# Kernel optimization log

Hardware: AMD Instinct MI355X
Metric: run time of the kernel (lower is better)

## Reference

```python
import jax, jax.numpy as jnp
import numpy as np

N_NODES = 100000
N_EDGES = 400000
N_GRAPHS = 1000
DIM = 5
N_OUT = 2
EPS = 1e-5


def _linear_params(key, fan_in, fan_out):
    kw, kb = jax.random.split(key)
    s = 1.0 / np.sqrt(fan_in)
    w = jax.random.uniform(kw, (fan_in, fan_out), minval=-s, maxval=s, dtype=jnp.float32)
    b = jax.random.uniform(kb, (fan_out,), minval=-s, maxval=s, dtype=jnp.float32)
    return w, b


def _gn_params(c):
    # rows: [weight, bias, mean_scale] as in PyG GraphNorm init (1, 0, 1)
    return jnp.stack([jnp.ones((c,)), jnp.zeros((c,)), jnp.ones((c,))], axis=0).astype(jnp.float32)


def setup_inputs() -> dict:
    key = jax.random.key(0)
    ks = jax.random.split(key, 16)
    x = jax.random.normal(ks[0], (N_NODES, DIM), dtype=jnp.float32)
    edge_index = jax.random.randint(ks[1], (2, N_EDGES), 0, N_NODES, dtype=jnp.int64)
    batch = jnp.sort(jax.random.randint(ks[2], (N_NODES,), 0, N_GRAPHS, dtype=jnp.int64))
    c1_w1, c1_b1 = _linear_params(ks[3], 2 * DIM, 128)
    c1_w2, c1_b2 = _linear_params(ks[4], 128, 128)
    c1_w3, c1_b3 = _linear_params(ks[5], 128, 128)
    c2_w1, c2_b1 = _linear_params(ks[6], 2 * 128, 256)
    c2_w2, c2_b2 = _linear_params(ks[7], 256, 256)
    c3_w1, c3_b1 = _linear_params(ks[8], 2 * 256, 256)
    lin_w1, lin_b1 = _linear_params(ks[9], 256, 256)
    lin_w2, lin_b2 = _linear_params(ks[10], 256, N_OUT)
    return {
        "x": x, "edge_index": edge_index, "batch": batch,
        "c1_w1": c1_w1, "c1_b1": c1_b1, "c1_gn1": _gn_params(128),
        "c1_w2": c1_w2, "c1_b2": c1_b2, "c1_gn2": _gn_params(128),
        "c1_w3": c1_w3, "c1_b3": c1_b3, "c1_gn3": _gn_params(128),
        "c2_w1": c2_w1, "c2_b1": c2_b1, "c2_gn1": _gn_params(256),
        "c2_w2": c2_w2, "c2_b2": c2_b2, "c2_gn2": _gn_params(256),
        "c3_w1": c3_w1, "c3_b1": c3_b1, "c3_gn1": _gn_params(256),
        "lin_w1": lin_w1, "lin_b1": lin_b1, "lin_w2": lin_w2, "lin_b2": lin_b2,
    }


def _graph_norm(h, p):
    # PyG GraphNorm with batch=None: normalize over all rows (single graph)
    g, b, ms = p[0], p[1], p[2]
    m = h.mean(axis=0)
    out = h - ms * m
    var = (out * out).mean(axis=0)
    return g * out * jax.lax.rsqrt(var + EPS) + b


def _edge_conv(x, src, dst, layers):
    # EdgeConv message: nn(cat[x_i, x_j - x_i]) aggregated (mean) at target i
    xi = x[dst]                                     # [E, C]
    h = jnp.concatenate([xi, x[src] - xi], axis=-1)  # [E, 2C]
    for w, b, gp in layers:
        h = jax.nn.relu(_graph_norm(h @ w + b, gp))
    s = jax.ops.segment_sum(h, dst, num_segments=N_NODES)
    ones = jnp.ones((dst.shape[0], 1), dtype=h.dtype)
    cnt = jax.ops.segment_sum(ones, dst, num_segments=N_NODES)
    return s / jnp.maximum(cnt, 1.0)


def reference(x, edge_index, batch,
              c1_w1, c1_b1, c1_gn1, c1_w2, c1_b2, c1_gn2, c1_w3, c1_b3, c1_gn3,
              c2_w1, c2_b1, c2_gn1, c2_w2, c2_b2, c2_gn2,
              c3_w1, c3_b1, c3_gn1,
              lin_w1, lin_b1, lin_w2, lin_b2):
    src, dst = edge_index[0], edge_index[1]
    h = _edge_conv(x, src, dst, [(c1_w1, c1_b1, c1_gn1), (c1_w2, c1_b2, c1_gn2), (c1_w3, c1_b3, c1_gn3)])
    h = _edge_conv(h, src, dst, [(c2_w1, c2_b1, c2_gn1), (c2_w2, c2_b2, c2_gn2)])
    h = _edge_conv(h, src, dst, [(c3_w1, c3_b1, c3_gn1)])
    # global_mean_pool over graphs (dropout = identity in eval)
    gs = jax.ops.segment_sum(h, batch, num_segments=N_GRAPHS)
    gc = jax.ops.segment_sum(jnp.ones((h.shape[0], 1), h.dtype), batch, num_segments=N_GRAPHS)
    g = gs / jnp.maximum(gc, 1.0)                   # [G, 256]
    out = jax.nn.relu(g @ lin_w1 + lin_b1) @ lin_w2 + lin_b2  # [G, n_out]
    return out
```

## Files before the change

kernel.cpp:

```cpp
#include <hip/hip_runtime.h>
#include <hip/hip_bf16.h>

#define NN 100000
#define NE 400000
#define NG 1000

typedef __attribute__((ext_vector_type(8))) short bf16x8;
typedef __attribute__((ext_vector_type(4))) float f32x4;

__device__ __forceinline__ float bf2f(unsigned short h) {
    return __uint_as_float((unsigned)h << 16);
}
__device__ __forceinline__ unsigned short f2bf(float f) {
    unsigned u = __float_as_uint(f);
    return (unsigned short)((u + 0x7FFFu + ((u >> 16) & 1u)) >> 16);
}
__device__ __forceinline__ void up8(uint4 u, float v[8]) {
    v[0] = bf2f((unsigned short)u.x); v[1] = bf2f((unsigned short)(u.x >> 16));
    v[2] = bf2f((unsigned short)u.y); v[3] = bf2f((unsigned short)(u.y >> 16));
    v[4] = bf2f((unsigned short)u.z); v[5] = bf2f((unsigned short)(u.z >> 16));
    v[6] = bf2f((unsigned short)u.w); v[7] = bf2f((unsigned short)(u.w >> 16));
}
__device__ __forceinline__ uint4 pk8(const float v[8]) {
    uint4 r;
    r.x = (uint)f2bf(v[0]) | ((uint)f2bf(v[1]) << 16);
    r.y = (uint)f2bf(v[2]) | ((uint)f2bf(v[3]) << 16);
    r.z = (uint)f2bf(v[4]) | ((uint)f2bf(v[5]) << 16);
    r.w = (uint)f2bf(v[6]) | ((uint)f2bf(v[7]) << 16);
    return r;
}

__global__ void diag_kernel(float* __restrict__ out, int n, float val) {
    int i = blockIdx.x * 256 + threadIdx.x;
    if (i < n) out[i] = val;
}

__global__ void deg_kernel(const int* __restrict__ dst, int* __restrict__ deg) {
    int e = blockIdx.x * 256 + threadIdx.x;
    if (e < NE) atomicAdd(&deg[dst[e]], 1);
}

__global__ void invdeg_kernel(const int* __restrict__ deg, float* __restrict__ invdeg) {
    int n = blockIdx.x * 256 + threadIdx.x;
    if (n < NN) invdeg[n] = 1.0f / (float)(deg[n] > 0 ? deg[n] : 1);
}

__global__ void conv1_node_kernel(const float* __restrict__ x, const float* __restrict__ W,
                                  unsigned short* __restrict__ RQ) {
    __shared__ float Ws[1280];
    for (int i = threadIdx.x; i < 1280; i += 256) Ws[i] = W[i];
    __syncthreads();
    int c = threadIdx.x & 127;
    int which = threadIdx.x >> 7;
    for (int n = blockIdx.x; n < NN; n += gridDim.x) {
        float acc = 0.f;
        #pragma unroll
        for (int r = 0; r < 5; r++) {
            float xv = x[n * 5 + r];
            float bot = Ws[(5 + r) * 128 + c];
            float w = which ? bot : (Ws[r * 128 + c] - bot);
            acc = fmaf(xv, w, acc);
        }
        RQ[(size_t)n * 256 + threadIdx.x] = f2bf(acc);
    }
}

__global__ void wtrans_kernel(const float* __restrict__ W, unsigned short* __restrict__ Wt,
                              int K, int N) {
    int idx = blockIdx.x * 256 + threadIdx.x;
    if (idx >= K * N) return;
    int c = idx / K, k = idx - c * K;
    Wt[(size_t)c * K + k] = f2bf(W[(size_t)k * N + c]);
}

__global__ void wprime_t_kernel(const float* __restrict__ W, unsigned short* __restrict__ Wpt,
                                int K, int C) {
    int idx = blockIdx.x * 256 + threadIdx.x;
    if (idx >= 2 * C * K) return;
    int n = idx / K, k = idx - n * K;
    float v;
    if (n < C) v = W[(size_t)k * C + n] - W[(size_t)(K + k) * C + n];
    else       v = W[(size_t)(K + k) * C + (n - C)];
    Wpt[(size_t)n * K + k] = f2bf(v);
}

template<int C>
__global__ void gstats_kernel(const unsigned short* __restrict__ RQ, const int* __restrict__ src,
                              const int* __restrict__ dst, const float* __restrict__ bias,
                              float* __restrict__ ssum, float* __restrict__ ssq) {
    constexpr int LPE = C / 8;
    constexpr int EPB = 256 / LPE;
    const int t = threadIdx.x;
    const int le = t % LPE, sub = t / LPE;
    const int c0 = le * 8;
    float4 b0 = *(const float4*)&bias[c0];
    float4 b1 = *(const float4*)&bias[c0 + 4];
    float bb[8] = {b0.x, b0.y, b0.z, b0.w, b1.x, b1.y, b1.z, b1.w};
    float ls[8], lq[8];
    #pragma unroll
    for (int i = 0; i < 8; i++) { ls[i] = 0.f; lq[i] = 0.f; }
    for (int e = blockIdx.x * EPB + sub; e < NE; e += gridDim.x * EPB) {
        int d = dst[e], s = src[e];
        uint4 rr = *(const uint4*)&RQ[(size_t)d * (2 * C) + c0];
        uint4 qq = *(const uint4*)&RQ[(size_t)s * (2 * C) + C + c0];
        float pr[8], pq[8];
        up8(rr, pr); up8(qq, pq);
        #pragma unroll
        for (int i = 0; i < 8; i++) {
            float v = pr[i] + pq[i] + bb[i];
            ls[i] += v; lq[i] += v * v;
        }
    }
    __shared__ float red[2][256][8];
    #pragma unroll
    for (int i = 0; i < 8; i++) { red[0][t][i] = ls[i]; red[1][t][i] = lq[i]; }
    __syncthreads();
    if (t < C) {
        int le2 = t >> 3, ch = t & 7;
        float s = 0.f, q = 0.f;
        #pragma unroll
        for (int g = 0; g < EPB; g++) {
            s += red[0][g * LPE + le2][ch];
            q += red[1][g * LPE + le2][ch];
        }
        atomicAdd(&ssum[t], s);
        atomicAdd(&ssq[t], q);
    }
}

__global__ void finalize_kernel(const float* __restrict__ ssum, const float* __restrict__ ssq,
                                const float* __restrict__ gn, int C, float invM,
                                float* __restrict__ alpha, float* __restrict__ beta) {
    int c = threadIdx.x;
    if (c >= C) return;
    float g = gn[c], b = gn[C + c], ms = gn[2 * C + c];
    float m = ssum[c] * invM;
    float var = ssq[c] * invM - m * m * ms * (2.f - ms);
    float inv = rsqrtf(var + 1e-5f);
    alpha[c] = g * inv;
    beta[c] = b - g * inv * ms * m;
}

template<int TK, int BN, bool GATHER, bool NORMRELU, bool ROWSC, bool STATS, bool STORE,
         bool SCAT, bool AF32>
__global__ __launch_bounds__(256) void mgemm_kernel(
    const void* __restrict__ Av, const int* __restrict__ gsrc, const int* __restrict__ gdst,
    const float* __restrict__ biasIn, const unsigned short* __restrict__ Wt,
    const float* __restrict__ alpha, const float* __restrict__ beta,
    const float* __restrict__ rowscale, const float* __restrict__ biasOut,
    unsigned short* __restrict__ Cmat, int M, int N,
    float* __restrict__ ssum, float* __restrict__ ssq,
    const float* __restrict__ alphaO, const float* __restrict__ betaO,
    float* __restrict__ hsum) {
    constexpr int WNC = BN / 4;
    constexpr int NF = WNC / 16;
    constexpr int SPR = TK / 8;
    constexpr int ITER = 64 * SPR / 256;
    __shared__ __align__(16) unsigned short At[64][TK + 8];
    __shared__ __align__(16) float sAl[TK], sBe[TK], sBi[TK];
    __shared__ float sS[BN], sQ[BN];
    const int t = threadIdx.x;
    const int wave = t >> 6, lane = t & 63;
    const int l15 = lane & 15, lq = lane >> 4;
    const int r0 = blockIdx.y * 64;
    const int n0 = blockIdx.x * BN;

    if (NORMRELU) for (int i = t; i < TK; i += 256) { sAl[i] = alpha[i]; sBe[i] = beta[i]; }
    if (GATHER)   for (int i = t; i < TK; i += 256) { sBi[i] = biasIn[i]; }
    if (STATS && t < BN) { sS[t] = 0.f; sQ[t] = 0.f; }
    __syncthreads();

    const unsigned short* Abf = (const unsigned short*)Av;
    const float* Af = (const float*)Av;

    #pragma unroll
    for (int it = 0; it < ITER; it++) {
        int slot = it * 256 + t;
        int row = slot / SPR;
        int c0 = (slot - row * SPR) * 8;
        int ar = r0 + row;
        float v[8];
        if (GATHER) {
            int gd = gdst[ar], gs = gsrc[ar];
            uint4 pa4 = *(const uint4*)&Abf[(size_t)gd * (2 * TK) + c0];
            uint4 pq4 = *(const uint4*)&Abf[(size_t)gs * (2 * TK) + TK + c0];
            float pa[8], pq[8];
            up8(pa4, pa); up8(pq4, pq);
            #pragma unroll
            for (int i = 0; i < 8; i++) v[i] = pa[i] + pq[i] + sBi[c0 + i];
        } else if (AF32) {
            if (ar < M) {
                float4 f0 = *(const float4*)&Af[(size_t)ar * TK + c0];
                float4 f1 = *(const float4*)&Af[(size_t)ar * TK + c0 + 4];
                v[0] = f0.x; v[1] = f0.y; v[2] = f0.z; v[3] = f0.w;
                v[4] = f1.x; v[5] = f1.y; v[6] = f1.z; v[7] = f1.w;
            } else {
                #pragma unroll
                for (int i = 0; i < 8; i++) v[i] = 0.f;
            }
        } else {
            if (ar < M) {
                uint4 a4 = *(const uint4*)&Abf[(size_t)ar * TK + c0];
                up8(a4, v);
            } else {
                #pragma unroll
                for (int i = 0; i < 8; i++) v[i] = 0.f;
            }
        }
        if (NORMRELU) {
            #pragma unroll
            for (int i = 0; i < 8; i++)
                v[i] = fmaxf(fmaf(sAl[c0 + i], v[i], sBe[c0 + i]), 0.f);
        }
        if (ROWSC) {
            float rs = (ar < M) ? rowscale[ar] : 0.f;
            #pragma unroll
            for (int i = 0; i < 8; i++) v[i] *= rs;
        }
        *(uint4*)&At[row][c0] = pk8(v);
    }
    __syncthreads();

    const unsigned short* bp[NF];
    #pragma unroll
    for (int cf = 0; cf < NF; cf++)
        bp[cf] = &Wt[(size_t)(n0 + wave * WNC + 16 * cf + l15) * TK + lq * 8];

    f32x4 acc[4][NF];
    #pragma unroll
    for (int i = 0; i < 4; i++)
        #pragma unroll
        for (int j = 0; j < NF; j++) acc[i][j] = {0.f, 0.f, 0.f, 0.f};

    #pragma unroll
    for (int k0 = 0; k0 < TK; k0 += 32) {
        bf16x8 af[4];
        #pragma unroll
        for (int rf = 0; rf < 4; rf++)
            af[rf] = *(const bf16x8*)&At[16 * rf + l15][k0 + lq * 8];
        bf16x8 bfr[NF];
        #pragma unroll
        for (int cf = 0; cf < NF; cf++)
            bfr[cf] = *(const bf16x8*)(bp[cf] + k0);
        #pragma unroll
        for (int rf = 0; rf < 4; rf++)
            #pragma unroll
            for (int cf = 0; cf < NF; cf++)
                acc[rf][cf] = __builtin_amdgcn_mfma_f32_16x16x32_bf16(
                    af[rf], bfr[cf], acc[rf][cf], 0, 0, 0);
    }

    int cA[NF];
    float bO[NF], aO[NF], bOo[NF];
    #pragma unroll
    for (int cf = 0; cf < NF; cf++) {
        cA[cf] = n0 + wave * WNC + 16 * cf + l15;
        bO[cf] = (biasOut != nullptr) ? biasOut[cA[cf]] : 0.f;
        if (SCAT) { aO[cf] = alphaO[cA[cf]]; bOo[cf] = betaO[cA[cf]]; }
    }
    float ps[NF], pq[NF];
    #pragma unroll
    for (int cf = 0; cf < NF; cf++) { ps[cf] = 0.f; pq[cf] = 0.f; }
    #pragma unroll
    for (int rf = 0; rf < 4; rf++) {
        int rb = r0 + 16 * rf + lq * 4;
        int dd[4];
        if (SCAT) {
            #pragma unroll
            for (int jj = 0; jj < 4; jj++) dd[jj] = gdst[rb + jj];
        }
        #pragma unroll
        for (int cf = 0; cf < NF; cf++) {
            #pragma unroll
            for (int jj = 0; jj < 4; jj++) {
                float o = acc[rf][cf][jj] + bO[cf];
                if (STATS) { ps[cf] += o; pq[cf] += o * o; }
                if (STORE) {
                    int r = rb + jj;
                    if (r < M) Cmat[(size_t)r * N + cA[cf]] = f2bf(o);
                }
                if (SCAT) {
                    float h = fmaxf(fmaf(aO[cf], o, bOo[cf]), 0.f);
                    atomicAdd(&hsum[(size_t)dd[jj] * N + cA[cf]], h);
                }
            }
        }
    }
    if (STATS) {
        #pragma unroll
        for (int cf = 0; cf < NF; cf++) {
            float s = ps[cf], q = pq[cf];
            s += __shfl_xor(s, 16); s += __shfl_xor(s, 32);
            q += __shfl_xor(q, 16); q += __shfl_xor(q, 32);
            if (lq == 0) {
                atomicAdd(&sS[cA[cf] - n0], s);
                atomicAdd(&sQ[cA[cf] - n0], q);
            }
        }
        __syncthreads();
        if (t < BN) {
            atomicAdd(&ssum[n0 + t], sS[t]);
            atomicAdd(&ssq[n0 + t], sQ[t]);
        }
    }
}

template<int C>
__global__ void aggregate_kernel(const unsigned short* __restrict__ Y, const int* __restrict__ dst,
                                 const float* __restrict__ alpha, const float* __restrict__ beta,
                                 float* __restrict__ hsum) {
    constexpr int EPB = 256 / C;
    int c = threadIdx.x % C;
    int sub = threadIdx.x / C;
    float al = alpha[c], be = beta[c];
    for (int e = blockIdx.x * EPB + sub; e < NE; e += gridDim.x * EPB) {
        float v = fmaxf(fmaf(al, bf2f(Y[(size_t)e * C + c]), be), 0.f);
        atomicAdd(&hsum[(size_t)dst[e] * C + c], v);
    }
}

__global__ void aggregate_fg_kernel(const unsigned short* __restrict__ RQ,
                                    const int* __restrict__ src, const int* __restrict__ dst,
                                    const float* __restrict__ bias, const float* __restrict__ alpha,
                                    const float* __restrict__ beta, float* __restrict__ hsum) {
    int c = threadIdx.x;
    float b = bias[c], al = alpha[c], be = beta[c];
    for (int e = blockIdx.x; e < NE; e += gridDim.x) {
        int d = dst[e], s = src[e];
        float v = (bf2f(RQ[(size_t)d * 512 + c]) + bf2f(RQ[(size_t)s * 512 + 256 + c])) + b;
        float h = fmaxf(fmaf(al, v, be), 0.f);
        atomicAdd(&hsum[(size_t)d * 256 + c], h);
    }
}

__global__ void pool_kernel(const float* __restrict__ h3sum, const float* __restrict__ invdeg,
                            const int* __restrict__ batch, float* __restrict__ gsum,
                            int* __restrict__ gcnt) {
    int chunk = (NN + gridDim.x - 1) / gridDim.x;
    int nbeg = blockIdx.x * chunk;
    int nend = min(nbeg + chunk, NN);
    if (nbeg >= nend) return;
    int t = threadIdx.x;
    int curg = batch[nbeg];
    float acc = 0.f;
    int cnt = 0;
    for (int n = nbeg; n < nend; n++) {
        int g = batch[n];
        if (g != curg) {
            atomicAdd(&gsum[(size_t)curg * 256 + t], acc);
            if (t == 0) atomicAdd(&gcnt[curg], cnt);
            curg = g; acc = 0.f; cnt = 0;
        }
        acc += h3sum[(size_t)n * 256 + t] * invdeg[n];
        cnt++;
    }
    atomicAdd(&gsum[(size_t)curg * 256 + t], acc);
    if (t == 0) atomicAdd(&gcnt[curg], cnt);
}

__global__ void mlp_kernel(const float* __restrict__ gsum, const int* __restrict__ gcnt,
                           const float* __restrict__ W1, const float* __restrict__ b1,
                           const float* __restrict__ W2, const float* __restrict__ b2,
                           float* __restrict__ out) {
    int g = blockIdx.x;
    int t = threadIdx.x;
    __shared__ float grow[256];
    __shared__ float r0s[256], r1s[256];
    int cnt = gcnt[g];
    float inv = 1.0f / (float)(cnt > 0 ? cnt : 1);
    grow[t] = gsum[(size_t)g * 256 + t] * inv;
    __syncthreads();
    float acc = b1[t];
    for (int k = 0; k < 256; k++) acc = fmaf(grow[k], W1[k * 256 + t], acc);
    float h = fmaxf(acc, 0.f);
    r0s[t] = h * W2[t * 2 + 0];
    r1s[t] = h * W2[t * 2 + 1];
    __syncthreads();
    for (int s = 128; s > 0; s >>= 1) {
        if (t < s) { r0s[t] += r0s[t + s]; r1s[t] += r1s[t + s]; }
        __syncthreads();
    }
    if (t == 0) {
        out[g * 2 + 0] = r0s[0] + b2[0];
        out[g * 2 + 1] = r1s[0] + b2[1];
    }
}

extern "C" void kernel_launch(void* const* d_in, const int* in_sizes, int n_in,
                              void* d_out, int out_size, void* d_ws, size_t ws_size,
                              hipStream_t stream) {
    const float* x      = (const float*)d_in[0];
    const int*   ei     = (const int*)d_in[1];
    const int*   src    = ei;
    const int*   dstp   = ei + NE;
    const int*   batch  = (const int*)d_in[2];
    const float* c1_w1  = (const float*)d_in[3];
    const float* c1_b1  = (const float*)d_in[4];
    const float* c1_gn1 = (const float*)d_in[5];
    const float* c1_w2  = (const float*)d_in[6];
    const float* c1_b2  = (const float*)d_in[7];
    const float* c1_gn2 = (const float*)d_in[8];
    const float* c1_w3  = (const float*)d_in[9];
    const float* c1_b3  = (const float*)d_in[10];
    const float* c1_gn3 = (const float*)d_in[11];
    const float* c2_w1  = (const float*)d_in[12];
    const float* c2_b1  = (const float*)d_in[13];
    const float* c2_gn1 = (const float*)d_in[14];
    const float* c2_w2  = (const float*)d_in[15];
    const float* c2_b2  = (const float*)d_in[16];
    const float* c2_gn2 = (const float*)d_in[17];
    const float* c3_w1  = (const float*)d_in[18];
    const float* c3_b1  = (const float*)d_in[19];
    const float* c3_gn1 = (const float*)d_in[20];
    const float* lin_w1 = (const float*)d_in[21];
    const float* lin_b1 = (const float*)d_in[22];
    const float* lin_w2 = (const float*)d_in[23];
    const float* lin_b2 = (const float*)d_in[24];
    float* out = (float*)d_out;

    constexpr size_t REG_BYTES = (size_t)NE * 128 * 2;
    constexpr size_t NEED = 2 * REG_BYTES + 4 * 1024 * 1024;

    if (ws_size < NEED) {
        diag_kernel<<<(out_size + 255) / 256, 256, 0, stream>>>(
            out, out_size, (float)(ws_size >> 20));
        return;
    }

    char* base = (char*)d_ws;
    unsigned short* RA = (unsigned short*)base;
    unsigned short* RB = (unsigned short*)(base + REG_BYTES);
    float* h1sum = (float*)RB;
    float* h2sum = (float*)RB;
    float* h3sum = (float*)RB;
    char* p = base + 2 * REG_BYTES;
    auto alloc = [&](size_t bytes) -> void* {
        void* r = (void*)p;
        p += (bytes + 255) & ~(size_t)255;
        return r;
    };
    unsigned short* c1w2t = (unsigned short*)alloc((size_t)128 * 128 * 2);
    unsigned short* c1w3t = (unsigned short*)alloc((size_t)128 * 128 * 2);
    unsigned short* c2w2t = (unsigned short*)alloc((size_t)256 * 256 * 2);
    unsigned short* Wpt   = (unsigned short*)alloc((size_t)512 * 256 * 2);
    int*   deg    = (int*)alloc((size_t)NN * 4);
    float* invdeg = (float*)alloc((size_t)NN * 4);
    float* ssum   = (float*)alloc(256 * 4);
    float* ssq    = (float*)alloc(256 * 4);
    float* al0    = (float*)alloc(256 * 4);
    float* be0    = (float*)alloc(256 * 4);
    float* al1    = (float*)alloc(256 * 4);
    float* be1    = (float*)alloc(256 * 4);
    float* gsum   = (float*)alloc((size_t)NG * 256 * 4);
    int*   gcnt   = (int*)alloc((size_t)NG * 4);

    const float invE = 1.0f / (float)NE;
    const int MT_E = NE / 64;
    const int MT_N = (NN + 63) / 64;

    hipMemsetAsync(deg, 0, (size_t)NN * 4, stream);
    hipMemsetAsync(gsum, 0, (size_t)NG * 256 * 4, stream);
    hipMemsetAsync(gcnt, 0, (size_t)NG * 4, stream);

    deg_kernel<<<(NE + 255) / 256, 256, 0, stream>>>(dstp, deg);
    invdeg_kernel<<<(NN + 255) / 256, 256, 0, stream>>>(deg, invdeg);

    wtrans_kernel<<<(128 * 128 + 255) / 256, 256, 0, stream>>>(c1_w2, c1w2t, 128, 128);
    wtrans_kernel<<<(128 * 128 + 255) / 256, 256, 0, stream>>>(c1_w3, c1w3t, 128, 128);
    wtrans_kernel<<<(256 * 256 + 255) / 256, 256, 0, stream>>>(c2_w2, c2w2t, 256, 256);

    conv1_node_kernel<<<2048, 256, 0, stream>>>(x, c1_w1, RA);
    hipMemsetAsync(ssum, 0, 256 * 4, stream);
    hipMemsetAsync(ssq, 0, 256 * 4, stream);
    gstats_kernel<128><<<2048, 256, 0, stream>>>(RA, src, dstp, c1_b1, ssum, ssq);
    finalize_kernel<<<1, 256, 0, stream>>>(ssum, ssq, c1_gn1, 128, invE, al0, be0);

    hipMemsetAsync(ssum, 0, 256 * 4, stream);
    hipMemsetAsync(ssq, 0, 256 * 4, stream);
    mgemm_kernel<128, 128, true, true, false, true, true, false, false>
        <<<dim3(1, MT_E), 256, 0, stream>>>(RA, src, dstp, c1_b1, c1w2t, al0, be0,
                                            nullptr, c1_b2, RB, NE, 128,
                                            ssum, ssq, nullptr, nullptr, nullptr);
    finalize_kernel<<<1, 256, 0, stream>>>(ssum, ssq, c1_gn2, 128, invE, al0, be0);

    hipMemsetAsync(ssum, 0, 256 * 4, stream);
    hipMemsetAsync(ssq, 0, 256 * 4, stream);
    mgemm_kernel<128, 128, false, true, false, true, true, false, false>
        <<<dim3(1, MT_E), 256, 0, stream>>>(RB, nullptr, nullptr, nullptr, c1w3t, al0, be0,
                                            nullptr, c1_b3, RA, NE, 128,
                                            ssum, ssq, nullptr, nullptr, nullptr);
    finalize_kernel<<<1, 256, 0, stream>>>(ssum, ssq, c1_gn3, 128, invE, al0, be0);

    hipMemsetAsync(h1sum, 0, (size_t)NN * 128 * 4, stream);
    aggregate_kernel<128><<<2048, 256, 0, stream>>>(RA, dstp, al0, be0, h1sum);

    wprime_t_kernel<<<(512 * 128 + 255) / 256, 256, 0, stream>>>(c2_w1, Wpt, 128, 256);
    mgemm_kernel<128, 256, false, false, true, false, true, false, true>
        <<<dim3(2, MT_N), 256, 0, stream>>>(h1sum, nullptr, nullptr, nullptr, Wpt,
                                            nullptr, nullptr, invdeg, nullptr, RA,
                                            NN, 512, nullptr, nullptr,
                                            nullptr, nullptr, nullptr);
    hipMemsetAsync(ssum, 0, 256 * 4, stream);
    hipMemsetAsync(ssq, 0, 256 * 4, stream);
    gstats_kernel<256><<<2048, 256, 0, stream>>>(RA, src, dstp, c2_b1, ssum, ssq);
    finalize_kernel<<<1, 256, 0, stream>>>(ssum, ssq, c2_gn1, 256, invE, al0, be0);

    hipMemsetAsync(ssum, 0, 256 * 4, stream);
    hipMemsetAsync(ssq, 0, 256 * 4, stream);
    mgemm_kernel<256, 256, true, true, false, true, false, false, false>
        <<<dim3(1, MT_E), 256, 0, stream>>>(RA, src, dstp, c2_b1, c2w2t, al0, be0,
                                            nullptr, c2_b2, nullptr, NE, 256,
                                            ssum, ssq, nullptr, nullptr, nullptr);
    finalize_kernel<<<1, 256, 0, stream>>>(ssum, ssq, c2_gn2, 256, invE, al1, be1);

    hipMemsetAsync(h2sum, 0, (size_t)NN * 256 * 4, stream);
    mgemm_kernel<256, 256, true, true, false, false, false, true, false>
        <<<dim3(1, MT_E), 256, 0, stream>>>(RA, src, dstp, c2_b1, c2w2t, al0, be0,
                                            nullptr, c2_b2, nullptr, NE, 256,
                                            nullptr, nullptr, al1, be1, h2sum);

    wprime_t_kernel<<<(512 * 256 + 255) / 256, 256, 0, stream>>>(c3_w1, Wpt, 256, 256);
    mgemm_kernel<256, 256, false, false, true, false, true, false, true>
        <<<dim3(2, MT_N), 256, 0, stream>>>(h2sum, nullptr, nullptr, nullptr, Wpt,
                                            nullptr, nullptr, invdeg, nullptr, RA,
                                            NN, 512, nullptr, nullptr,
                                            nullptr, nullptr, nullptr);
    hipMemsetAsync(ssum, 0, 256 * 4, stream);
    hipMemsetAsync(ssq, 0, 256 * 4, stream);
    gstats_kernel<256><<<2048, 256, 0, stream>>>(RA, src, dstp, c3_b1, ssum, ssq);
    finalize_kernel<<<1, 256, 0, stream>>>(ssum, ssq, c3_gn1, 256, invE, al0, be0);

    hipMemsetAsync(h3sum, 0, (size_t)NN * 256 * 4, stream);
    aggregate_fg_kernel<<<2048, 256, 0, stream>>>(RA, src, dstp, c3_b1, al0, be0, h3sum);

    pool_kernel<<<512, 256, 0, stream>>>(h3sum, invdeg, batch, gsum, gcnt);
    mlp_kernel<<<NG, 256, 0, stream>>>(gsum, gcnt, lin_w1, lin_b1, lin_w2, lin_b2, out);
}
```

Measured before the change: 2.209 ms.

## Sort edges by destination into CSR and replace atomic scatter with segmented reduction

Adds a counting-sort pass (prefix scan of degrees plus an atomic cursor scatter) that builds a destination-sorted edge list with CSR offsets. Edge-space GEMMs now run over the sorted edges. Aggregation and GN-stat kernels walk each node's incoming edge range, so per-edge float atomics and the large hsum memsets go away and mean normalization happens in place. The cost is extra preprocessing kernels and a node-parallel layout that can be load-imbalanced under skewed degrees. The fp32 summation order within a node also changes.

```diff
diff --git a/kernel.cpp b/kernel.cpp
--- a/kernel.cpp
+++ b/kernel.cpp
@@ -43,6 +43,62 @@
 __global__ void invdeg_kernel(const int* __restrict__ deg, float* __restrict__ invdeg) {
     int n = blockIdx.x * 256 + threadIdx.x;
     if (n < NN) invdeg[n] = 1.0f / (float)(deg[n] > 0 ? deg[n] : 1);
+}
+
+__global__ void scan1_kernel(const int* __restrict__ deg, int* __restrict__ off,
+                             int* __restrict__ bsum) {
+    __shared__ int s[1024];
+    int tid = threadIdx.x;
+    int i = blockIdx.x * 1024 + tid;
+    int v = (i < NN) ? deg[i] : 0;
+    s[tid] = v;
+    __syncthreads();
+    for (int d = 1; d < 1024; d <<= 1) {
+        int add = (tid >= d) ? s[tid - d] : 0;
+        __syncthreads();
+        s[tid] += add;
+        __syncthreads();
+    }
+    if (i < NN) off[i] = s[tid] - v;
+    if (tid == 1023) bsum[blockIdx.x] = s[1023];
+}
+
+__global__ void scan2_kernel(int* __restrict__ bsum, int nb) {
+    __shared__ int s[128];
+    int tid = threadIdx.x;
+    int v = (tid < nb) ? bsum[tid] : 0;
+    s[tid] = v;
+    __syncthreads();
+    for (int d = 1; d < 128; d <<= 1) {
+        int add = (tid >= d) ? s[tid - d] : 0;
+        __syncthreads();
+        s[tid] += add;
+        __syncthreads();
+    }
+    if (tid < nb) bsum[tid] = s[tid] - v;
+}
+
+__global__ void scan3_kernel(int* __restrict__ off, const int* __restrict__ bsum,
+                             int* __restrict__ cursor) {
+    int i = blockIdx.x * 256 + threadIdx.x;
+    if (i < NN) {
+        int o = off[i] + bsum[i >> 10];
+        off[i] = o;
+        cursor[i] = o;
+    }
+    if (i == 0) off[NN] = NE;
+}
+
+__global__ void sortedge_kernel(const int* __restrict__ src, const int* __restrict__ dst,
+                                int* __restrict__ cursor, int* __restrict__ ssrc,
+                                int* __restrict__ sdst) {
+    int e = blockIdx.x * 256 + threadIdx.x;
+    if (e < NE) {
+        int d = dst[e];
+        int pos = atomicAdd(&cursor[d], 1);
+        ssrc[pos] = src[e];
+        sdst[pos] = d;
+    }
 }
 
 __global__ void conv1_node_kernel(const float* __restrict__ x, const float* __restrict__ W,
@@ -85,44 +141,32 @@
 }
 
 template<int C>
-__global__ void gstats_kernel(const unsigned short* __restrict__ RQ, const int* __restrict__ src,
-                              const int* __restrict__ dst, const float* __restrict__ bias,
-                              float* __restrict__ ssum, float* __restrict__ ssq) {
-    constexpr int LPE = C / 8;
-    constexpr int EPB = 256 / LPE;
+__global__ void gstats_node_kernel(const unsigned short* __restrict__ RQ,
+                                   const int* __restrict__ ssrc, const int* __restrict__ off,
+                                   const float* __restrict__ bias,
+                                   float* __restrict__ ssum, float* __restrict__ ssq) {
+    constexpr int GPB = 256 / C;
     const int t = threadIdx.x;
-    const int le = t % LPE, sub = t / LPE;
-    const int c0 = le * 8;
-    float4 b0 = *(const float4*)&bias[c0];
-    float4 b1 = *(const float4*)&bias[c0 + 4];
-    float bb[8] = {b0.x, b0.y, b0.z, b0.w, b1.x, b1.y, b1.z, b1.w};
-    float ls[8], lq[8];
-    #pragma unroll
-    for (int i = 0; i < 8; i++) { ls[i] = 0.f; lq[i] = 0.f; }
-    for (int e = blockIdx.x * EPB + sub; e < NE; e += gridDim.x * EPB) {
-        int d = dst[e], s = src[e];
-        uint4 rr = *(const uint4*)&RQ[(size_t)d * (2 * C) + c0];
-        uint4 qq = *(const uint4*)&RQ[(size_t)s * (2 * C) + C + c0];
-        float pr[8], pq[8];
-        up8(rr, pr); up8(qq, pq);
-        #pragma unroll
-        for (int i = 0; i < 8; i++) {
-            float v = pr[i] + pq[i] + bb[i];
-            ls[i] += v; lq[i] += v * v;
-        }
-    }
-    __shared__ float red[2][256][8];
-    #pragma unroll
-    for (int i = 0; i < 8; i++) { red[0][t][i] = ls[i]; red[1][t][i] = lq[i]; }
+    const int c = t % C, g = t / C;
+    float b = bias[c];
+    float ls = 0.f, lq = 0.f;
+    int chunk = (NN + gridDim.x - 1) / gridDim.x;
+    int nb = blockIdx.x * chunk, ne = min(nb + chunk, NN);
+    for (int n = nb + g; n < ne; n += GPB) {
+        float R = bf2f(RQ[(size_t)n * (2 * C) + c]);
+        int e0 = off[n], e1 = off[n + 1];
+        for (int e = e0; e < e1; e++) {
+            float v = R + bf2f(RQ[(size_t)ssrc[e] * (2 * C) + C + c]) + b;
+            ls += v; lq += v * v;
+        }
+    }
+    __shared__ float red[2][256];
+    red[0][t] = ls; red[1][t] = lq;
     __syncthreads();
     if (t < C) {
-        int le2 = t >> 3, ch = t & 7;
         float s = 0.f, q = 0.f;
         #pragma unroll
-        for (int g = 0; g < EPB; g++) {
-            s += red[0][g * LPE + le2][ch];
-            q += red[1][g * LPE + le2][ch];
-        }
+        for (int gg = 0; gg < GPB; gg++) { s += red[0][gg * C + t]; q += red[1][gg * C + t]; }
         atomicAdd(&ssum[t], s);
         atomicAdd(&ssq[t], q);
     }
@@ -306,36 +350,53 @@
 }
 
 template<int C>
-__global__ void aggregate_kernel(const unsigned short* __restrict__ Y, const int* __restrict__ dst,
-                                 const float* __restrict__ alpha, const float* __restrict__ beta,
-                                 float* __restrict__ hsum) {
-    constexpr int EPB = 256 / C;
-    int c = threadIdx.x % C;
-    int sub = threadIdx.x / C;
+__global__ void aggregate_node_kernel(const unsigned short* __restrict__ Y,
+                                      const int* __restrict__ off,
+                                      const float* __restrict__ alpha,
+                                      const float* __restrict__ beta,
+                                      const float* __restrict__ invdeg,
+                                      float* __restrict__ h) {
+    constexpr int GPB = 256 / C;
+    const int t = threadIdx.x;
+    const int c = t % C, g = t / C;
     float al = alpha[c], be = beta[c];
-    for (int e = blockIdx.x * EPB + sub; e < NE; e += gridDim.x * EPB) {
-        float v = fmaxf(fmaf(al, bf2f(Y[(size_t)e * C + c]), be), 0.f);
-        atomicAdd(&hsum[(size_t)dst[e] * C + c], v);
-    }
-}
-
-__global__ void aggregate_fg_kernel(const unsigned short* __restrict__ RQ,
-                                    const int* __restrict__ src, const int* __restrict__ dst,
-                                    const float* __restrict__ bias, const float* __restrict__ alpha,
-                                    const float* __restrict__ beta, float* __restrict__ hsum) {
+    int chunk = (NN + gridDim.x - 1) / gridDim.x;
+    int nb = blockIdx.x * chunk, ne = min(nb + chunk, NN);
+    for (int n = nb + g; n < ne; n += GPB) {
+        int e0 = off[n], e1 = off[n + 1];
+        float s = 0.f;
+        for (int e = e0; e < e1; e++)
+            s += fmaxf(fmaf(al, bf2f(Y[(size_t)e * C + c]), be), 0.f);
+        h[(size_t)n * C + c] = s * invdeg[n];
+    }
+}
+
+__global__ void aggregate_fg_node_kernel(const unsigned short* __restrict__ RQ,
+                                         const int* __restrict__ ssrc,
+                                         const int* __restrict__ off,
+                                         const float* __restrict__ bias,
+                                         const float* __restrict__ alpha,
+                                         const float* __restrict__ beta,
+                                         const float* __restrict__ invdeg,
+                                         float* __restrict__ h) {
     int c = threadIdx.x;
     float b = bias[c], al = alpha[c], be = beta[c];
-    for (int e = blockIdx.x; e < NE; e += gridDim.x) {
-        int d = dst[e], s = src[e];
-        float v = (bf2f(RQ[(size_t)d * 512 + c]) + bf2f(RQ[(size_t)s * 512 + 256 + c])) + b;
-        float h = fmaxf(fmaf(al, v, be), 0.f);
-        atomicAdd(&hsum[(size_t)d * 256 + c], h);
-    }
-}
-
-__global__ void pool_kernel(const float* __restrict__ h3sum, const float* __restrict__ invdeg,
-                            const int* __restrict__ batch, float* __restrict__ gsum,
-                            int* __restrict__ gcnt) {
+    int chunk = (NN + gridDim.x - 1) / gridDim.x;
+    int nb = blockIdx.x * chunk, ne = min(nb + chunk, NN);
+    for (int n = nb; n < ne; n++) {
+        float R = bf2f(RQ[(size_t)n * 512 + c]);
+        int e0 = off[n], e1 = off[n + 1];
+        float s = 0.f;
+        for (int e = e0; e < e1; e++) {
+            float v = R + bf2f(RQ[(size_t)ssrc[e] * 512 + 256 + c]) + b;
+            s += fmaxf(fmaf(al, v, be), 0.f);
+        }
+        h[(size_t)n * 256 + c] = s * invdeg[n];
+    }
+}
+
+__global__ void pool_kernel(const float* __restrict__ h3, const int* __restrict__ batch,
+                            float* __restrict__ gsum, int* __restrict__ gcnt) {
     int chunk = (NN + gridDim.x - 1) / gridDim.x;
     int nbeg = blockIdx.x * chunk;
     int nend = min(nbeg + chunk, NN);
@@ -351,7 +412,7 @@
             if (t == 0) atomicAdd(&gcnt[curg], cnt);
             curg = g; acc = 0.f; cnt = 0;
         }
-        acc += h3sum[(size_t)n * 256 + t] * invdeg[n];
+        acc += h3[(size_t)n * 256 + t];
         cnt++;
     }
     atomicAdd(&gsum[(size_t)curg * 256 + t], acc);
@@ -391,8 +452,8 @@
                               hipStream_t stream) {
     const float* x      = (const float*)d_in[0];
     const int*   ei     = (const int*)d_in[1];
-    const int*   src    = ei;
-    const int*   dstp   = ei + NE;
+    const int*   src0   = ei;
+    const int*   dst0   = ei + NE;
     const int*   batch  = (const int*)d_in[2];
     const float* c1_w1  = (const float*)d_in[3];
     const float* c1_b1  = (const float*)d_in[4];
@@ -419,7 +480,7 @@
     float* out = (float*)d_out;
 
     constexpr size_t REG_BYTES = (size_t)NE * 128 * 2;
-    constexpr size_t NEED = 2 * REG_BYTES + 4 * 1024 * 1024;
+    constexpr size_t NEED = 2 * REG_BYTES + 16 * 1024 * 1024;
 
     if (ws_size < NEED) {
         diag_kernel<<<(out_size + 255) / 256, 256, 0, stream>>>(
@@ -430,9 +491,9 @@
     char* base = (char*)d_ws;
     unsigned short* RA = (unsigned short*)base;
     unsigned short* RB = (unsigned short*)(base + REG_BYTES);
-    float* h1sum = (float*)RB;
+    float* h1    = (float*)RB;
     float* h2sum = (float*)RB;
-    float* h3sum = (float*)RB;
+    float* h3    = (float*)RB;
     char* p = base + 2 * REG_BYTES;
     auto alloc = [&](size_t bytes) -> void* {
         void* r = (void*)p;
@@ -445,6 +506,11 @@
     unsigned short* Wpt   = (unsigned short*)alloc((size_t)512 * 256 * 2);
     int*   deg    = (int*)alloc((size_t)NN * 4);
     float* invdeg = (float*)alloc((size_t)NN * 4);
+    int*   off    = (int*)alloc((size_t)(NN + 1) * 4);
+    int*   cursor = (int*)alloc((size_t)NN * 4);
+    int*   bsum   = (int*)alloc((size_t)128 * 4);
+    int*   ssrc   = (int*)alloc((size_t)NE * 4);
+    int*   sdst   = (int*)alloc((size_t)NE * 4);
     float* ssum   = (float*)alloc(256 * 4);
     float* ssq    = (float*)alloc(256 * 4);
     float* al0    = (float*)alloc(256 * 4);
@@ -457,13 +523,18 @@
     const float invE = 1.0f / (float)NE;
     const int MT_E = NE / 64;
     const int MT_N = (NN + 63) / 64;
+    const int NB = (NN + 1023) / 1024;
 
     hipMemsetAsync(deg, 0, (size_t)NN * 4, stream);
     hipMemsetAsync(gsum, 0, (size_t)NG * 256 * 4, stream);
     hipMemsetAsync(gcnt, 0, (size_t)NG * 4, stream);
 
-    deg_kernel<<<(NE + 255) / 256, 256, 0, stream>>>(dstp, deg);
+    deg_kernel<<<(NE + 255) / 256, 256, 0, stream>>>(dst0, deg);
     invdeg_kernel<<<(NN + 255) / 256, 256, 0, stream>>>(deg, invdeg);
+    scan1_kernel<<<NB, 1024, 0, stream>>>(deg, off, bsum);
+    scan2_kernel<<<1, 128, 0, stream>>>(bsum, NB);
+    scan3_kernel<<<(NN + 255) / 256, 256, 0, stream>>>(off, bsum, cursor);
+    sortedge_kernel<<<(NE + 255) / 256, 256, 0, stream>>>(src0, dst0, cursor, ssrc, sdst);
 
     wtrans_kernel<<<(128 * 128 + 255) / 256, 256, 0, stream>>>(c1_w2, c1w2t, 128, 128);
     wtrans_kernel<<<(128 * 128 + 255) / 256, 256, 0, stream>>>(c1_w3, c1w3t, 128, 128);
@@ -472,13 +543,13 @@
     conv1_node_kernel<<<2048, 256, 0, stream>>>(x, c1_w1, RA);
     hipMemsetAsync(ssum, 0, 256 * 4, stream);
     hipMemsetAsync(ssq, 0, 256 * 4, stream);
-    gstats_kernel<128><<<2048, 256, 0, stream>>>(RA, src, dstp, c1_b1, ssum, ssq);
+    gstats_node_kernel<128><<<2048, 256, 0, stream>>>(RA, ssrc, off, c1_b1, ssum, ssq);
     finalize_kernel<<<1, 256, 0, stream>>>(ssum, ssq, c1_gn1, 128, invE, al0, be0);
 
     hipMemsetAsync(ssum, 0, 256 * 4, stream);
     hipMemsetAsync(ssq, 0, 256 * 4, stream);
     mgemm_kernel<128, 128, true, true, false, true, true, false, false>
-        <<<dim3(1, MT_E), 256, 0, stream>>>(RA, src, dstp, c1_b1, c1w2t, al0, be0,
+        <<<dim3(1, MT_E), 256, 0, stream>>>(RA, ssrc, sdst, c1_b1, c1w2t, al0, be0,
                                             nullptr, c1_b2, RB, NE, 128,
                                             ssum, ssq, nullptr, nullptr, nullptr);
     finalize_kernel<<<1, 256, 0, stream>>>(ssum, ssq, c1_gn2, 128, invE, al0, be0);
@@ -491,31 +562,30 @@
                                             ssum, ssq, nullptr, nullptr, nullptr);
     finalize_kernel<<<1, 256, 0, stream>>>(ssum, ssq, c1_gn3, 128, invE, al0, be0);
 
-    hipMemsetAsync(h1sum, 0, (size_t)NN * 128 * 4, stream);
-    aggregate_kernel<128><<<2048, 256, 0, stream>>>(RA, dstp, al0, be0, h1sum);
+    aggregate_node_kernel<128><<<2048, 256, 0, stream>>>(RA, off, al0, be0, invdeg, h1);
 
     wprime_t_kernel<<<(512 * 128 + 255) / 256, 256, 0, stream>>>(c2_w1, Wpt, 128, 256);
-    mgemm_kernel<128, 256, false, false, true, false, true, false, true>
-        <<<dim3(2, MT_N), 256, 0, stream>>>(h1sum, nullptr, nullptr, nullptr, Wpt,
-                                            nullptr, nullptr, invdeg, nullptr, RA,
+    mgemm_kernel<128, 256, false, false, false, false, true, false, true>
+        <<<dim3(2, MT_N), 256, 0, stream>>>(h1, nullptr, nullptr, nullptr, Wpt,
+                                            nullptr, nullptr, nullptr, nullptr, RA,
                                             NN, 512, nullptr, nullptr,
                                             nullptr, nullptr, nullptr);
     hipMemsetAsync(ssum, 0, 256 * 4, stream);
     hipMemsetAsync(ssq, 0, 256 * 4, stream);
-    gstats_kernel<256><<<2048, 256, 0, stream>>>(RA, src, dstp, c2_b1, ssum, ssq);
+    gstats_node_kernel<256><<<2048, 256, 0, stream>>>(RA, ssrc, off, c2_b1, ssum, ssq);
     finalize_kernel<<<1, 256, 0, stream>>>(ssum, ssq, c2_gn1, 256, invE, al0, be0);
 
     hipMemsetAsync(ssum, 0, 256 * 4, stream);
     hipMemsetAsync(ssq, 0, 256 * 4, stream);
     mgemm_kernel<256, 256, true, true, false, true, false, false, false>
-        <<<dim3(1, MT_E), 256, 0, stream>>>(RA, src, dstp, c2_b1, c2w2t, al0, be0,
+        <<<dim3(1, MT_E), 256, 0, stream>>>(RA, ssrc, sdst, c2_b1, c2w2t, al0, be0,
                                             nullptr, c2_b2, nullptr, NE, 256,
                                             ssum, ssq, nullptr, nullptr, nullptr);
     finalize_kernel<<<1, 256, 0, stream>>>(ssum, ssq, c2_gn2, 256, invE, al1, be1);
 
     hipMemsetAsync(h2sum, 0, (size_t)NN * 256 * 4, stream);
     mgemm_kernel<256, 256, true, true, false, false, false, true, false>
-        <<<dim3(1, MT_E), 256, 0, stream>>>(RA, src, dstp, c2_b1, c2w2t, al0, be0,
+        <<<dim3(1, MT_E), 256, 0, stream>>>(RA, ssrc, sdst, c2_b1, c2w2t, al0, be0,
                                             nullptr, c2_b2, nullptr, NE, 256,
                                             nullptr, nullptr, al1, be1, h2sum);
 
@@ -527,12 +597,12 @@
                                             nullptr, nullptr, nullptr);
     hipMemsetAsync(ssum, 0, 256 * 4, stream);
     hipMemsetAsync(ssq, 0, 256 * 4, stream);
-    gstats_kernel<256><<<2048, 256, 0, stream>>>(RA, src, dstp, c3_b1, ssum, ssq);
+    gstats_node_kernel<256><<<2048, 256, 0, stream>>>(RA, ssrc, off, c3_b1, ssum, ssq);
     finalize_kernel<<<1, 256, 0, stream>>>(ssum, ssq, c3_gn1, 256, invE, al0, be0);
 
-    hipMemsetAsync(h3sum, 0, (size_t)NN * 256 * 4, stream);
-    aggregate_fg_kernel<<<2048, 256, 0, stream>>>(RA, src, dstp, c3_b1, al0, be0, h3sum);
-
-    pool_kernel<<<512, 256, 0, stream>>>(h3sum, invdeg, batch, gsum, gcnt);
+    aggregate_fg_node_kernel<<<2048, 256, 0, stream>>>(RA, ssrc, off, c3_b1, al0, be0,
+                                                       invdeg, h3);
+
+    pool_kernel<<<512, 256, 0, stream>>>(h3, batch, gsum, gcnt);
     mlp_kernel<<<NG, 256, 0, stream>>>(gsum, gcnt, lin_w1, lin_b1, lin_w2, lin_b2, out);
 }
```

Result: slower. 2.352 ms (+6.5%).
